# Optimization experiments

Hardware: AMD Instinct MI355X
Metric: run time of the kernel (lower is better)

The kernel has to match this reference:

```python
import jax, jax.numpy as jnp
import numpy as np

NUM_HEADS = 16
DIM_HEAD = 64
DIM = 1024
SCALE = DIM ** (-0.5)  # NOTE: source scales by model dim, not dim_head


def setup_inputs() -> dict:
    key = jax.random.key(0)
    ks = jax.random.split(key, 6)
    b, n, d = 2, 2048, DIM
    return {
        "x": jax.random.normal(ks[0], (b, n, d), dtype=jnp.float32),
        "mask": jnp.ones((b, n), dtype=bool),
        "Wq": jax.random.normal(ks[1], (NUM_HEADS * DIM_HEAD, d), dtype=jnp.float32) * 0.02,
        "Wk": jax.random.normal(ks[2], (DIM_HEAD, d), dtype=jnp.float32) * 0.02,
        "Wv": jax.random.normal(ks[3], (DIM_HEAD, d), dtype=jnp.float32) * 0.02,
        "Wfc": jax.random.normal(ks[4], (d, NUM_HEADS * DIM_HEAD), dtype=jnp.float32) * 0.02,
        "bfc": jnp.zeros((d,), dtype=jnp.float32),
    }


def reference(x, mask, Wq, Wk, Wv, Wfc, bfc):
    b, n, _ = x.shape
    # projections (nn.Linear: y = x @ W.T)
    q = (x @ Wq.T).reshape(b, n, NUM_HEADS, DIM_HEAD).transpose(0, 2, 1, 3)  # b h n d
    k = x @ Wk.T  # b n d  (single shared MQA head)
    v = x @ Wv.T  # b n d
    energy = jnp.einsum("bhid,bjd->bhij", q, k) * SCALE  # b h i j
    mask_value = -jnp.finfo(energy.dtype).max
    # input mask: k_mask is all ones in source, so only query rows are masked
    q_mask = mask[:, None, :, None]  # b 1 i 1
    energy = jnp.where(q_mask, energy, mask_value)
    # causal mask: positions j > i are masked (i == j since self-attention)
    i = jnp.arange(n)
    causal = i[:, None] < i[None, :]  # True where future
    energy = jnp.where(causal[None, None, :, :], mask_value, energy)
    attn = jax.nn.softmax(energy, axis=-1)
    # dropout_rate = 0.0 -> identity
    out = jnp.einsum("bhij,bjd->bhid", attn, v)
    out = out.transpose(0, 2, 1, 3).reshape(b, n, NUM_HEADS * DIM_HEAD)
    return out @ Wfc.T + bfc
```

## Files before the change

### kernel.cpp

```cpp
#include <hip/hip_runtime.h>
#include <math.h>

#define NH 16
#define DH 64
#define DM 1024
#define NS 2048
#define BB 2
#define MR (BB * NS)
#define LDQ 1152
#define C_EXP 0.0450842201f

typedef unsigned short u16;
typedef __attribute__((ext_vector_type(8))) short short8;
typedef __attribute__((ext_vector_type(4))) float floatx4;
typedef __attribute__((ext_vector_type(4))) u16 u16x4;

#if __has_builtin(__builtin_amdgcn_exp2f)
#define EXP2(x) __builtin_amdgcn_exp2f(x)
#else
#define EXP2(x) exp2f(x)
#endif

static __device__ __forceinline__ u16 f2bf(float f) {
  union { float f; unsigned u; } v; v.f = f;
  unsigned r = v.u + 0x7fffu + ((v.u >> 16) & 1u);
  return (u16)(r >> 16);
}
static __device__ __forceinline__ u16 f2bf_fast(float f) {
  union { float f; unsigned u; } v; v.f = f;
  return (u16)((v.u + 0x8000u) >> 16);
}

#define GLDS16(gp, lp)                                                        \
  __builtin_amdgcn_global_load_lds(                                           \
      (const __attribute__((address_space(1))) void*)(const void*)(gp),       \
      (__attribute__((address_space(3))) void*)(void*)(lp), 16, 0, 0)

__global__ __launch_bounds__(256) void cast_all(
    const float* __restrict__ x, const float* __restrict__ wq,
    const float* __restrict__ wk, const float* __restrict__ wv,
    const float* __restrict__ wfc, u16* __restrict__ xb,
    u16* __restrict__ wqkvb, u16* __restrict__ wfcb) {
  const int NX = MR * DM / 4, NQ = DM * DM / 4, NK = DH * DM / 4;
  int id = blockIdx.x * 256 + threadIdx.x;
  const float* src;
  u16* dst;
  int off;
  if (id < NX) { src = x; dst = xb; off = id; }
  else if (id < NX + NQ) { src = wq; dst = wqkvb; off = id - NX; }
  else if (id < NX + NQ + NK) { src = wk; dst = wqkvb + (size_t)DM * DM; off = id - NX - NQ; }
  else if (id < NX + NQ + 2 * NK) { src = wv; dst = wqkvb + (size_t)(DM + DH) * DM; off = id - NX - NQ - NK; }
  else { src = wfc; dst = wfcb; off = id - NX - NQ - 2 * NK; }
  float4 f = ((const float4*)src)[off];
  u16x4 o;
  o[0] = f2bf(f.x); o[1] = f2bf(f.y); o[2] = f2bf(f.z); o[3] = f2bf(f.w);
  ((u16x4*)dst)[off] = o;
}

__global__ __launch_bounds__(64) void gemm_bf16(
    const u16* __restrict__ A, const u16* __restrict__ W,
    const float* __restrict__ bias, void* __restrict__ Cout,
    u16* __restrict__ vT, int M, int N, int K, int ldc, int out_bf16,
    int v_bx) {
  __shared__ u16 As[2][64 * 32];
  __shared__ u16 Ws[2][64 * 32];
  const int lane = threadIdx.x;
  const int lr = lane & 15, quad = lane >> 4;
  const int m0 = blockIdx.y * 64, n0 = blockIdx.x * 64;

  const u16* gA[4];
  const u16* gW[4];
#pragma unroll
  for (int g = 0; g < 4; ++g) {
    int ci = g * 64 + lane;
    int row = ci >> 2;
    int cg = (ci & 3) ^ ((row >> 1) & 3);
    gA[g] = A + (size_t)(m0 + row) * K + cg * 8;
    gW[g] = W + (size_t)(n0 + row) * K + cg * 8;
  }

  floatx4 acc[4][4] = {};
  const int nt = K >> 5;

#pragma unroll
  for (int g = 0; g < 4; ++g) GLDS16(gA[g], &As[0][g * 512]);
#pragma unroll
  for (int g = 0; g < 4; ++g) GLDS16(gW[g], &Ws[0][g * 512]);

  for (int t = 0; t < nt; ++t) {
    if (t + 1 < nt) {
      const int ko = (t + 1) << 5;
      const int nb = (t + 1) & 1;
#pragma unroll
      for (int g = 0; g < 4; ++g) GLDS16(gA[g] + ko, &As[nb][g * 512]);
#pragma unroll
      for (int g = 0; g < 4; ++g) GLDS16(gW[g] + ko, &Ws[nb][g * 512]);
      asm volatile("s_waitcnt vmcnt(8)" ::: "memory");
    } else {
      asm volatile("s_waitcnt vmcnt(0)" ::: "memory");
    }
    const u16* as = As[t & 1];
    const u16* ws = Ws[t & 1];
    short8 af[4], wf[4];
#pragma unroll
    for (int mi = 0; mi < 4; ++mi) {
      int rr = mi * 16 + lr;
      af[mi] = *(const short8*)&as[rr * 32 + ((quad ^ ((rr >> 1) & 3)) << 3)];
    }
#pragma unroll
    for (int nj = 0; nj < 4; ++nj) {
      int rc = nj * 16 + lr;
      wf[nj] = *(const short8*)&ws[rc * 32 + ((quad ^ ((rc >> 1) & 3)) << 3)];
    }
#pragma unroll
    for (int mi = 0; mi < 4; ++mi)
#pragma unroll
      for (int nj = 0; nj < 4; ++nj)
        acc[mi][nj] = __builtin_amdgcn_mfma_f32_16x16x32_bf16(
            af[mi], wf[nj], acc[mi][nj], 0, 0, 0);
  }

  if (vT && blockIdx.x == v_bx) {
#pragma unroll
    for (int mi = 0; mi < 4; ++mi)
#pragma unroll
      for (int nj = 0; nj < 4; ++nj)
#pragma unroll
        for (int r = 0; r < 4; ++r)
          vT[(size_t)(nj * 16 + lr) * MR + m0 + mi * 16 + quad * 4 + r] =
              f2bf(acc[mi][nj][r]);
    return;
  }

#pragma unroll
  for (int mi = 0; mi < 4; ++mi) {
#pragma unroll
    for (int nj = 0; nj < 4; ++nj) {
      int col = n0 + nj * 16 + lr;
      float badd = bias ? bias[col] : 0.f;
#pragma unroll
      for (int r = 0; r < 4; ++r) {
        int row = m0 + mi * 16 + quad * 4 + r;
        float v = acc[mi][nj][r] + badd;
        if (out_bf16)
          ((u16*)Cout)[(size_t)row * ldc + col] = f2bf(v);
        else
          ((float*)Cout)[(size_t)row * ldc + col] = v;
      }
    }
  }
}

__global__ __launch_bounds__(128) void attn_mfma(
    const u16* __restrict__ qkv,
    const u16* __restrict__ vT,
    u16* __restrict__ aob) {
  __shared__ u16 Ks[2][64 * 64];
  __shared__ u16 Vt[2][64 * 64];
  __shared__ u16 Ps[2][16 * 72];

  const int b = blockIdx.z;
  const int p = blockIdx.x;
  const int head = blockIdx.y;
  const int tid = threadIdx.x;
  const int lane = tid & 63;
  const int lr = lane & 15, quad = lane >> 4;
  const int w = tid >> 6;
  const size_t rowb = (size_t)b * NS;
  const u16* kvK = qkv + rowb * LDQ + 1024;
  const u16* vTb = vT + rowb;

  int srow[4], scg[4];
#pragma unroll
  for (int g = 0; g < 4; ++g) {
    int ci = w * 256 + g * 64 + lane;
    srow[g] = ci >> 3;
    scg[g] = (ci & 7) ^ (srow[g] & 7);
  }

  for (int phase = 0; phase < 2; ++phase) {
    const int s = (phase == 0) ? (63 - p) : p;
    const int i0q = s * 32;
    const int ntp = (s >> 1) + 1;
    const int irow = i0q + w * 16 + quad * 4;

    const u16* qp = qkv + (rowb + i0q + w * 16 + lr) * LDQ + head * DH;
    short8 aq0 = *(const short8*)(qp + quad * 8);
    short8 aq1 = *(const short8*)(qp + 32 + quad * 8);

    floatx4 o[4] = {};
    float lacc[4] = {0.f, 0.f, 0.f, 0.f};

#pragma unroll
    for (int g = 0; g < 4; ++g)
      GLDS16(kvK + (size_t)srow[g] * LDQ + scg[g] * 8,
             &Ks[0][(w * 256 + g * 64) * 8]);
#pragma unroll
    for (int g = 0; g < 4; ++g)
      GLDS16(vTb + (size_t)srow[g] * MR + scg[g] * 8,
             &Vt[0][(w * 256 + g * 64) * 8]);

    for (int t = 0; t < ntp; ++t) {
      const int buf = t & 1;
      __syncthreads();

      if (t + 1 < ntp) {
        const int j0n = (t + 1) * 64;
        const int nb2 = buf ^ 1;
#pragma unroll
        for (int g = 0; g < 4; ++g)
          GLDS16(kvK + (size_t)(j0n + srow[g]) * LDQ + scg[g] * 8,
                 &Ks[nb2][(w * 256 + g * 64) * 8]);
#pragma unroll
        for (int g = 0; g < 4; ++g)
          GLDS16(vTb + (size_t)srow[g] * MR + j0n + scg[g] * 8,
                 &Vt[nb2][(w * 256 + g * 64) * 8]);
      }

      const int j0 = t * 64;
      const u16* ksb = Ks[buf];
      const u16* vtb = Vt[buf];
      floatx4 sv[4];
#pragma unroll
      for (int jb = 0; jb < 4; ++jb) {
        const int krow = jb * 16 + lr;
        short8 bk0 = *(const short8*)&ksb[krow * 64 + ((quad ^ (krow & 7)) << 3)];
        short8 bk1 = *(const short8*)&ksb[krow * 64 + (((4 + quad) ^ (krow & 7)) << 3)];
        floatx4 z = {};
        z = __builtin_amdgcn_mfma_f32_16x16x32_bf16(aq0, bk0, z, 0, 0, 0);
        z = __builtin_amdgcn_mfma_f32_16x16x32_bf16(aq1, bk1, z, 0, 0, 0);
        sv[jb] = z;
      }

      u16* Pw = Ps[w];
      const bool lastt = (t == ntp - 1);
#pragma unroll
      for (int jb = 0; jb < 4; ++jb) {
#pragma unroll
        for (int r = 0; r < 4; ++r) {
          float pe = EXP2(sv[jb][r] * C_EXP);
          if (lastt && (j0 + jb * 16 + lr > irow + r)) pe = 0.f;
          lacc[r] += pe;
          const int row = quad * 4 + r, colj = jb * 16 + lr;
          Pw[row * 72 + ((((colj >> 3) + (row >> 1)) & 7) << 3) + (colj & 7)] =
              f2bf_fast(pe);
        }
      }
      asm volatile("s_waitcnt lgkmcnt(0)" ::: "memory");
      short8 ap0 = *(const short8*)&Pw[lr * 72 + (((quad + (lr >> 1)) & 7) << 3)];
      short8 ap1 = *(const short8*)&Pw[lr * 72 + (((4 + quad + (lr >> 1)) & 7) << 3)];

#pragma unroll
      for (int nb = 0; nb < 4; ++nb) {
        const int d0 = nb * 16 + lr;
        short8 bv0 = *(const short8*)&vtb[d0 * 64 + ((quad ^ (d0 & 7)) << 3)];
        short8 bv1 = *(const short8*)&vtb[d0 * 64 + (((4 + quad) ^ (d0 & 7)) << 3)];
        o[nb] = __builtin_amdgcn_mfma_f32_16x16x32_bf16(ap0, bv0, o[nb], 0, 0, 0);
        o[nb] = __builtin_amdgcn_mfma_f32_16x16x32_bf16(ap1, bv1, o[nb], 0, 0, 0);
      }
    }

#pragma unroll
    for (int r = 0; r < 4; ++r) {
      float l = lacc[r];
      l += __shfl_xor(l, 1);
      l += __shfl_xor(l, 2);
      l += __shfl_xor(l, 4);
      l += __shfl_xor(l, 8);
      lacc[r] = l;
    }
#pragma unroll
    for (int nb = 0; nb < 4; ++nb)
#pragma unroll
      for (int r = 0; r < 4; ++r)
        aob[(rowb + irow + r) * DM + head * DH + nb * 16 + lr] =
            f2bf(o[nb][r] / lacc[r]);

    __syncthreads();
  }
}

extern "C" void kernel_launch(void* const* d_in, const int* in_sizes, int n_in,
                              void* d_out, int out_size, void* d_ws, size_t ws_size,
                              hipStream_t stream) {
  const float* x = (const float*)d_in[0];
  const float* Wq = (const float*)d_in[2];
  const float* Wk = (const float*)d_in[3];
  const float* Wv = (const float*)d_in[4];
  const float* Wfc = (const float*)d_in[5];
  const float* bfc = (const float*)d_in[6];

  u16* xb = (u16*)d_ws;
  u16* wqkvb = xb + (size_t)MR * DM;
  u16* wfcb = wqkvb + (size_t)LDQ * DM;
  u16* qkv = wfcb + (size_t)DM * DM;
  u16* vT = qkv + (size_t)MR * LDQ;
  u16* aob = xb;

  cast_all<<<dim3((MR * DM + DM * DM * 2 + DH * DM * 2) / 1024), dim3(256), 0,
             stream>>>(x, Wq, Wk, Wv, Wfc, xb, wqkvb, wfcb);
  gemm_bf16<<<dim3(LDQ / 64, MR / 64), dim3(64), 0, stream>>>(
      xb, wqkvb, nullptr, qkv, vT, MR, LDQ, DM, LDQ, 1, 17);
  attn_mfma<<<dim3(32, NH, BB), dim3(128), 0, stream>>>(qkv, vT, aob);
  gemm_bf16<<<dim3(DM / 64, MR / 64), dim3(64), 0, stream>>>(
      aob, wfcb, bfc, d_out, nullptr, MR, DM, DM, DM, 0, -1);
}
```

Baseline: 185.8 us.

## Load GEMM and attention operands directly from global into registers, bypassing LDS

Both GEMM kernels now load MFMA fragments straight from global memory into registers, using a two-step register double buffer instead of LDS staging with global_load_lds. The grid is also transposed so consecutive blocks walk along M. The attention kernel becomes one wave per block handling 32 query rows, and reads K and V^T fragments directly from global, keeping LDS only for the P tile. This removes LDS traffic and barriers but relies on the caches to serve repeated K/V and weight reads, so loads become uncoalesced, 16-byte-per-lane strided accesses.

```diff
diff --git a/kernel.cpp b/kernel.cpp
--- a/kernel.cpp
+++ b/kernel.cpp
@@ -21,6 +21,8 @@
 #define EXP2(x) exp2f(x)
 #endif
 
+#define MFMA16(a, b, c) __builtin_amdgcn_mfma_f32_16x16x32_bf16((a), (b), (c), 0, 0, 0)
+
 static __device__ __forceinline__ u16 f2bf(float f) {
   union { float f; unsigned u; } v; v.f = f;
   unsigned r = v.u + 0x7fffu + ((v.u >> 16) & 1u);
@@ -30,11 +32,6 @@
   union { float f; unsigned u; } v; v.f = f;
   return (u16)((v.u + 0x8000u) >> 16);
 }
-
-#define GLDS16(gp, lp)                                                        \
-  __builtin_amdgcn_global_load_lds(                                           \
-      (const __attribute__((address_space(1))) void*)(const void*)(gp),       \
-      (__attribute__((address_space(3))) void*)(void*)(lp), 16, 0, 0)
 
 __global__ __launch_bounds__(256) void cast_all(
     const float* __restrict__ x, const float* __restrict__ wq,
@@ -57,70 +54,57 @@
   ((u16x4*)dst)[off] = o;
 }
 
-__global__ __launch_bounds__(64) void gemm_bf16(
+__global__ __launch_bounds__(64) void gemm_dl(
     const u16* __restrict__ A, const u16* __restrict__ W,
     const float* __restrict__ bias, void* __restrict__ Cout,
     u16* __restrict__ vT, int M, int N, int K, int ldc, int out_bf16,
-    int v_bx) {
-  __shared__ u16 As[2][64 * 32];
-  __shared__ u16 Ws[2][64 * 32];
+    int v_by) {
   const int lane = threadIdx.x;
   const int lr = lane & 15, quad = lane >> 4;
-  const int m0 = blockIdx.y * 64, n0 = blockIdx.x * 64;
-
-  const u16* gA[4];
-  const u16* gW[4];
-#pragma unroll
-  for (int g = 0; g < 4; ++g) {
-    int ci = g * 64 + lane;
-    int row = ci >> 2;
-    int cg = (ci & 3) ^ ((row >> 1) & 3);
-    gA[g] = A + (size_t)(m0 + row) * K + cg * 8;
-    gW[g] = W + (size_t)(n0 + row) * K + cg * 8;
-  }
-
+  const int m0 = blockIdx.x * 64, n0 = blockIdx.y * 64;
+
+  const u16* gA = A + (size_t)(m0 + lr) * K + quad * 8;
+  const u16* gW = W + (size_t)(n0 + lr) * K + quad * 8;
+
+  short8 afA[4], afB[4], wf[4];
   floatx4 acc[4][4] = {};
+
+#pragma unroll
+  for (int i = 0; i < 4; ++i) {
+    afA[i] = *(const short8*)(gA + (size_t)i * 16 * K);
+    wf[i] = *(const short8*)(gW + (size_t)i * 16 * K);
+  }
+
   const int nt = K >> 5;
-
-#pragma unroll
-  for (int g = 0; g < 4; ++g) GLDS16(gA[g], &As[0][g * 512]);
-#pragma unroll
-  for (int g = 0; g < 4; ++g) GLDS16(gW[g], &Ws[0][g * 512]);
-
-  for (int t = 0; t < nt; ++t) {
-    if (t + 1 < nt) {
-      const int ko = (t + 1) << 5;
-      const int nb = (t + 1) & 1;
-#pragma unroll
-      for (int g = 0; g < 4; ++g) GLDS16(gA[g] + ko, &As[nb][g * 512]);
-#pragma unroll
-      for (int g = 0; g < 4; ++g) GLDS16(gW[g] + ko, &Ws[nb][g * 512]);
-      asm volatile("s_waitcnt vmcnt(8)" ::: "memory");
-    } else {
-      asm volatile("s_waitcnt vmcnt(0)" ::: "memory");
-    }
-    const u16* as = As[t & 1];
-    const u16* ws = Ws[t & 1];
-    short8 af[4], wf[4];
-#pragma unroll
-    for (int mi = 0; mi < 4; ++mi) {
-      int rr = mi * 16 + lr;
-      af[mi] = *(const short8*)&as[rr * 32 + ((quad ^ ((rr >> 1) & 3)) << 3)];
-    }
+  for (int t = 0; t < nt; t += 2) {
+    const int k1 = (t + 1) << 5;
+    const int k2 = (t + 2) << 5;
+#pragma unroll
+    for (int i = 0; i < 4; ++i)
+      afB[i] = *(const short8*)(gA + (size_t)i * 16 * K + k1);
 #pragma unroll
     for (int nj = 0; nj < 4; ++nj) {
-      int rc = nj * 16 + lr;
-      wf[nj] = *(const short8*)&ws[rc * 32 + ((quad ^ ((rc >> 1) & 3)) << 3)];
-    }
-#pragma unroll
-    for (int mi = 0; mi < 4; ++mi)
-#pragma unroll
-      for (int nj = 0; nj < 4; ++nj)
-        acc[mi][nj] = __builtin_amdgcn_mfma_f32_16x16x32_bf16(
-            af[mi], wf[nj], acc[mi][nj], 0, 0, 0);
-  }
-
-  if (vT && blockIdx.x == v_bx) {
+#pragma unroll
+      for (int mi = 0; mi < 4; ++mi)
+        acc[mi][nj] = MFMA16(afA[mi], wf[nj], acc[mi][nj]);
+      wf[nj] = *(const short8*)(gW + (size_t)nj * 16 * K + k1);
+    }
+    const bool hn = (t + 2) < nt;
+    if (hn) {
+#pragma unroll
+      for (int i = 0; i < 4; ++i)
+        afA[i] = *(const short8*)(gA + (size_t)i * 16 * K + k2);
+    }
+#pragma unroll
+    for (int nj = 0; nj < 4; ++nj) {
+#pragma unroll
+      for (int mi = 0; mi < 4; ++mi)
+        acc[mi][nj] = MFMA16(afB[mi], wf[nj], acc[mi][nj]);
+      if (hn) wf[nj] = *(const short8*)(gW + (size_t)nj * 16 * K + k2);
+    }
+  }
+
+  if (v_by >= 0 && (int)blockIdx.y == v_by) {
 #pragma unroll
     for (int mi = 0; mi < 4; ++mi)
 #pragma unroll
@@ -151,132 +135,127 @@
   }
 }
 
-__global__ __launch_bounds__(128) void attn_mfma(
+__global__ __launch_bounds__(64) void attn_dl(
     const u16* __restrict__ qkv,
     const u16* __restrict__ vT,
     u16* __restrict__ aob) {
-  __shared__ u16 Ks[2][64 * 64];
-  __shared__ u16 Vt[2][64 * 64];
-  __shared__ u16 Ps[2][16 * 72];
-
-  const int b = blockIdx.z;
-  const int p = blockIdx.x;
-  const int head = blockIdx.y;
-  const int tid = threadIdx.x;
-  const int lane = tid & 63;
+  __shared__ u16 Ps[2][32 * 72];
+
+  const int b = blockIdx.z, p = blockIdx.x, head = blockIdx.y;
+  const int lane = threadIdx.x;
   const int lr = lane & 15, quad = lane >> 4;
-  const int w = tid >> 6;
   const size_t rowb = (size_t)b * NS;
-  const u16* kvK = qkv + rowb * LDQ + 1024;
-  const u16* vTb = vT + rowb;
-
-  int srow[4], scg[4];
-#pragma unroll
-  for (int g = 0; g < 4; ++g) {
-    int ci = w * 256 + g * 64 + lane;
-    srow[g] = ci >> 3;
-    scg[g] = (ci & 7) ^ (srow[g] & 7);
-  }
+  const u16* kp = qkv + (rowb + lr) * LDQ + 1024;
+  const u16* vp = vT + rowb + (size_t)lr * MR;
 
   for (int phase = 0; phase < 2; ++phase) {
     const int s = (phase == 0) ? (63 - p) : p;
     const int i0q = s * 32;
     const int ntp = (s >> 1) + 1;
-    const int irow = i0q + w * 16 + quad * 4;
-
-    const u16* qp = qkv + (rowb + i0q + w * 16 + lr) * LDQ + head * DH;
-    short8 aq0 = *(const short8*)(qp + quad * 8);
-    short8 aq1 = *(const short8*)(qp + 32 + quad * 8);
-
-    floatx4 o[4] = {};
-    float lacc[4] = {0.f, 0.f, 0.f, 0.f};
-
-#pragma unroll
-    for (int g = 0; g < 4; ++g)
-      GLDS16(kvK + (size_t)srow[g] * LDQ + scg[g] * 8,
-             &Ks[0][(w * 256 + g * 64) * 8]);
-#pragma unroll
-    for (int g = 0; g < 4; ++g)
-      GLDS16(vTb + (size_t)srow[g] * MR + scg[g] * 8,
-             &Vt[0][(w * 256 + g * 64) * 8]);
+
+    short8 aq[2][2];
+#pragma unroll
+    for (int g = 0; g < 2; ++g) {
+      const u16* qp = qkv + (rowb + i0q + g * 16 + lr) * LDQ + head * DH;
+      aq[g][0] = *(const short8*)(qp + quad * 8);
+      aq[g][1] = *(const short8*)(qp + 32 + quad * 8);
+    }
+
+    floatx4 o[2][4] = {};
+    float lacc[2][4] = {};
+    short8 kf[8], vf[8];
+
+#pragma unroll
+    for (int jb = 0; jb < 4; ++jb) {
+      kf[2 * jb] = *(const short8*)(kp + (size_t)(jb * 16) * LDQ + quad * 8);
+      kf[2 * jb + 1] = *(const short8*)(kp + (size_t)(jb * 16) * LDQ + 32 + quad * 8);
+    }
 
     for (int t = 0; t < ntp; ++t) {
-      const int buf = t & 1;
-      __syncthreads();
+      const int j0 = t * 64;
+#pragma unroll
+      for (int nb = 0; nb < 4; ++nb) {
+        vf[2 * nb] = *(const short8*)(vp + (size_t)(nb * 16) * MR + j0 + quad * 8);
+        vf[2 * nb + 1] = *(const short8*)(vp + (size_t)(nb * 16) * MR + j0 + 32 + quad * 8);
+      }
+
+      floatx4 sv[2][4];
+#pragma unroll
+      for (int jb = 0; jb < 4; ++jb) {
+        floatx4 z0 = {}, z1 = {};
+        z0 = MFMA16(aq[0][0], kf[2 * jb], z0);
+        z0 = MFMA16(aq[0][1], kf[2 * jb + 1], z0);
+        z1 = MFMA16(aq[1][0], kf[2 * jb], z1);
+        z1 = MFMA16(aq[1][1], kf[2 * jb + 1], z1);
+        sv[0][jb] = z0;
+        sv[1][jb] = z1;
+      }
 
       if (t + 1 < ntp) {
-        const int j0n = (t + 1) * 64;
-        const int nb2 = buf ^ 1;
-#pragma unroll
-        for (int g = 0; g < 4; ++g)
-          GLDS16(kvK + (size_t)(j0n + srow[g]) * LDQ + scg[g] * 8,
-                 &Ks[nb2][(w * 256 + g * 64) * 8]);
-#pragma unroll
-        for (int g = 0; g < 4; ++g)
-          GLDS16(vTb + (size_t)srow[g] * MR + j0n + scg[g] * 8,
-                 &Vt[nb2][(w * 256 + g * 64) * 8]);
-      }
-
-      const int j0 = t * 64;
-      const u16* ksb = Ks[buf];
-      const u16* vtb = Vt[buf];
-      floatx4 sv[4];
-#pragma unroll
-      for (int jb = 0; jb < 4; ++jb) {
-        const int krow = jb * 16 + lr;
-        short8 bk0 = *(const short8*)&ksb[krow * 64 + ((quad ^ (krow & 7)) << 3)];
-        short8 bk1 = *(const short8*)&ksb[krow * 64 + (((4 + quad) ^ (krow & 7)) << 3)];
-        floatx4 z = {};
-        z = __builtin_amdgcn_mfma_f32_16x16x32_bf16(aq0, bk0, z, 0, 0, 0);
-        z = __builtin_amdgcn_mfma_f32_16x16x32_bf16(aq1, bk1, z, 0, 0, 0);
-        sv[jb] = z;
-      }
-
-      u16* Pw = Ps[w];
+        const int j0n = j0 + 64;
+#pragma unroll
+        for (int jb = 0; jb < 4; ++jb) {
+          kf[2 * jb] = *(const short8*)(kp + (size_t)(j0n + jb * 16) * LDQ + quad * 8);
+          kf[2 * jb + 1] = *(const short8*)(kp + (size_t)(j0n + jb * 16) * LDQ + 32 + quad * 8);
+        }
+      }
+
+      u16* Pw = Ps[t & 1];
       const bool lastt = (t == ntp - 1);
 #pragma unroll
-      for (int jb = 0; jb < 4; ++jb) {
+      for (int g = 0; g < 2; ++g) {
+        const int irow = i0q + g * 16 + quad * 4;
+#pragma unroll
+        for (int jb = 0; jb < 4; ++jb)
+#pragma unroll
+          for (int r = 0; r < 4; ++r) {
+            float pe = EXP2(sv[g][jb][r] * C_EXP);
+            if (lastt && (j0 + jb * 16 + lr > irow + r)) pe = 0.f;
+            lacc[g][r] += pe;
+            const int row = g * 16 + quad * 4 + r, colj = jb * 16 + lr;
+            Pw[row * 72 + ((((colj >> 3) + (row >> 1)) & 7) << 3) + (colj & 7)] =
+                f2bf_fast(pe);
+          }
+      }
+      asm volatile("s_waitcnt lgkmcnt(0)" ::: "memory");
+      short8 ap[2][2];
+#pragma unroll
+      for (int g = 0; g < 2; ++g) {
+        const int row = g * 16 + lr;
+        ap[g][0] = *(const short8*)&Pw[row * 72 + (((quad + (row >> 1)) & 7) << 3)];
+        ap[g][1] = *(const short8*)&Pw[row * 72 + (((4 + quad + (row >> 1)) & 7) << 3)];
+      }
+
+#pragma unroll
+      for (int nb = 0; nb < 4; ++nb)
+#pragma unroll
+        for (int g = 0; g < 2; ++g) {
+          o[g][nb] = MFMA16(ap[g][0], vf[2 * nb], o[g][nb]);
+          o[g][nb] = MFMA16(ap[g][1], vf[2 * nb + 1], o[g][nb]);
+        }
+    }
+
+#pragma unroll
+    for (int g = 0; g < 2; ++g)
+#pragma unroll
+      for (int r = 0; r < 4; ++r) {
+        float l = lacc[g][r];
+        l += __shfl_xor(l, 1);
+        l += __shfl_xor(l, 2);
+        l += __shfl_xor(l, 4);
+        l += __shfl_xor(l, 8);
+        lacc[g][r] = l;
+      }
+#pragma unroll
+    for (int g = 0; g < 2; ++g)
+#pragma unroll
+      for (int nb = 0; nb < 4; ++nb)
 #pragma unroll
         for (int r = 0; r < 4; ++r) {
-          float pe = EXP2(sv[jb][r] * C_EXP);
-          if (lastt && (j0 + jb * 16 + lr > irow + r)) pe = 0.f;
-          lacc[r] += pe;
-          const int row = quad * 4 + r, colj = jb * 16 + lr;
-          Pw[row * 72 + ((((colj >> 3) + (row >> 1)) & 7) << 3) + (colj & 7)] =
-              f2bf_fast(pe);
+          const int row = i0q + g * 16 + quad * 4 + r;
+          aob[(rowb + row) * DM + head * DH + nb * 16 + lr] =
+              f2bf(o[g][nb][r] / lacc[g][r]);
         }
-      }
-      asm volatile("s_waitcnt lgkmcnt(0)" ::: "memory");
-      short8 ap0 = *(const short8*)&Pw[lr * 72 + (((quad + (lr >> 1)) & 7) << 3)];
-      short8 ap1 = *(const short8*)&Pw[lr * 72 + (((4 + quad + (lr >> 1)) & 7) << 3)];
-
-#pragma unroll
-      for (int nb = 0; nb < 4; ++nb) {
-        const int d0 = nb * 16 + lr;
-        short8 bv0 = *(const short8*)&vtb[d0 * 64 + ((quad ^ (d0 & 7)) << 3)];
-        short8 bv1 = *(const short8*)&vtb[d0 * 64 + (((4 + quad) ^ (d0 & 7)) << 3)];
-        o[nb] = __builtin_amdgcn_mfma_f32_16x16x32_bf16(ap0, bv0, o[nb], 0, 0, 0);
-        o[nb] = __builtin_amdgcn_mfma_f32_16x16x32_bf16(ap1, bv1, o[nb], 0, 0, 0);
-      }
-    }
-
-#pragma unroll
-    for (int r = 0; r < 4; ++r) {
-      float l = lacc[r];
-      l += __shfl_xor(l, 1);
-      l += __shfl_xor(l, 2);
-      l += __shfl_xor(l, 4);
-      l += __shfl_xor(l, 8);
-      lacc[r] = l;
-    }
-#pragma unroll
-    for (int nb = 0; nb < 4; ++nb)
-#pragma unroll
-      for (int r = 0; r < 4; ++r)
-        aob[(rowb + irow + r) * DM + head * DH + nb * 16 + lr] =
-            f2bf(o[nb][r] / lacc[r]);
-
-    __syncthreads();
   }
 }
 
@@ -299,9 +278,9 @@
 
   cast_all<<<dim3((MR * DM + DM * DM * 2 + DH * DM * 2) / 1024), dim3(256), 0,
              stream>>>(x, Wq, Wk, Wv, Wfc, xb, wqkvb, wfcb);
-  gemm_bf16<<<dim3(LDQ / 64, MR / 64), dim3(64), 0, stream>>>(
+  gemm_dl<<<dim3(MR / 64, LDQ / 64), dim3(64), 0, stream>>>(
       xb, wqkvb, nullptr, qkv, vT, MR, LDQ, DM, LDQ, 1, 17);
-  attn_mfma<<<dim3(32, NH, BB), dim3(128), 0, stream>>>(qkv, vT, aob);
-  gemm_bf16<<<dim3(DM / 64, MR / 64), dim3(64), 0, stream>>>(
+  attn_dl<<<dim3(32, NH, BB), dim3(64), 0, stream>>>(qkv, vT, aob);
+  gemm_dl<<<dim3(MR / 64, DM / 64), dim3(64), 0, stream>>>(
       aob, wfcb, bfc, d_out, nullptr, MR, DM, DM, DM, 0, -1);
 }
```

After: 240.2 us. 1.29x slower.

## Split GEMM 64x64 tile across four waves and swap grid axes

Applied to the files above, without the earlier changes.

The projection GEMM kernel now uses 256 threads (four waves) per 64x64 output tile. Each wave computes a 32x32 quadrant, and each thread issues one async global-to-LDS load per operand per K-step, in place of one wave doing everything. The grid now walks M along x and N along y, which changes the block scheduling order so neighbouring blocks share weight tiles. This lowers per-wave register pressure and raises wave-level parallelism, but adds a __syncthreads per K iteration and relies on the barrier for completion of the async loads.

```diff
diff --git a/kernel.cpp b/kernel.cpp
--- a/kernel.cpp
+++ b/kernel.cpp
@@ -20,6 +20,8 @@
 #else
 #define EXP2(x) exp2f(x)
 #endif
+
+#define MFMA16(a, b, c) __builtin_amdgcn_mfma_f32_16x16x32_bf16((a), (b), (c), 0, 0, 0)
 
 static __device__ __forceinline__ u16 f2bf(float f) {
   union { float f; unsigned u; } v; v.f = f;
@@ -57,90 +59,80 @@
   ((u16x4*)dst)[off] = o;
 }
 
-__global__ __launch_bounds__(64) void gemm_bf16(
+__global__ __launch_bounds__(256) void gemm64(
     const u16* __restrict__ A, const u16* __restrict__ W,
     const float* __restrict__ bias, void* __restrict__ Cout,
     u16* __restrict__ vT, int M, int N, int K, int ldc, int out_bf16,
-    int v_bx) {
+    int v_by) {
   __shared__ u16 As[2][64 * 32];
   __shared__ u16 Ws[2][64 * 32];
-  const int lane = threadIdx.x;
+  const int tid = threadIdx.x;
+  const int lane = tid & 63;
   const int lr = lane & 15, quad = lane >> 4;
-  const int m0 = blockIdx.y * 64, n0 = blockIdx.x * 64;
-
-  const u16* gA[4];
-  const u16* gW[4];
-#pragma unroll
-  for (int g = 0; g < 4; ++g) {
-    int ci = g * 64 + lane;
-    int row = ci >> 2;
-    int cg = (ci & 3) ^ ((row >> 1) & 3);
-    gA[g] = A + (size_t)(m0 + row) * K + cg * 8;
-    gW[g] = W + (size_t)(n0 + row) * K + cg * 8;
-  }
-
-  floatx4 acc[4][4] = {};
+  const int wave = tid >> 6, wr = wave >> 1, wc = wave & 1;
+  const int m0 = blockIdx.x * 64, n0 = blockIdx.y * 64;
+
+  const int srow = tid >> 2;
+  const int scg = (tid & 3) ^ ((srow >> 1) & 3);
+  const u16* gA = A + (size_t)(m0 + srow) * K + scg * 8;
+  const u16* gW = W + (size_t)(n0 + srow) * K + scg * 8;
+  const int lo = wave * 512;
+
+  floatx4 acc[2][2] = {};
   const int nt = K >> 5;
 
-#pragma unroll
-  for (int g = 0; g < 4; ++g) GLDS16(gA[g], &As[0][g * 512]);
-#pragma unroll
-  for (int g = 0; g < 4; ++g) GLDS16(gW[g], &Ws[0][g * 512]);
+  GLDS16(gA, &As[0][lo]);
+  GLDS16(gW, &Ws[0][lo]);
 
   for (int t = 0; t < nt; ++t) {
+    __syncthreads();
     if (t + 1 < nt) {
       const int ko = (t + 1) << 5;
       const int nb = (t + 1) & 1;
-#pragma unroll
-      for (int g = 0; g < 4; ++g) GLDS16(gA[g] + ko, &As[nb][g * 512]);
-#pragma unroll
-      for (int g = 0; g < 4; ++g) GLDS16(gW[g] + ko, &Ws[nb][g * 512]);
-      asm volatile("s_waitcnt vmcnt(8)" ::: "memory");
-    } else {
-      asm volatile("s_waitcnt vmcnt(0)" ::: "memory");
+      GLDS16(gA + ko, &As[nb][lo]);
+      GLDS16(gW + ko, &Ws[nb][lo]);
     }
     const u16* as = As[t & 1];
     const u16* ws = Ws[t & 1];
-    short8 af[4], wf[4];
-#pragma unroll
-    for (int mi = 0; mi < 4; ++mi) {
-      int rr = mi * 16 + lr;
+    short8 af[2], wf[2];
+#pragma unroll
+    for (int mi = 0; mi < 2; ++mi) {
+      int rr = wr * 32 + mi * 16 + lr;
       af[mi] = *(const short8*)&as[rr * 32 + ((quad ^ ((rr >> 1) & 3)) << 3)];
     }
 #pragma unroll
-    for (int nj = 0; nj < 4; ++nj) {
-      int rc = nj * 16 + lr;
+    for (int nj = 0; nj < 2; ++nj) {
+      int rc = wc * 32 + nj * 16 + lr;
       wf[nj] = *(const short8*)&ws[rc * 32 + ((quad ^ ((rc >> 1) & 3)) << 3)];
     }
 #pragma unroll
-    for (int mi = 0; mi < 4; ++mi)
-#pragma unroll
-      for (int nj = 0; nj < 4; ++nj)
-        acc[mi][nj] = __builtin_amdgcn_mfma_f32_16x16x32_bf16(
-            af[mi], wf[nj], acc[mi][nj], 0, 0, 0);
-  }
-
-  if (vT && blockIdx.x == v_bx) {
-#pragma unroll
-    for (int mi = 0; mi < 4; ++mi)
-#pragma unroll
-      for (int nj = 0; nj < 4; ++nj)
+    for (int mi = 0; mi < 2; ++mi)
+#pragma unroll
+      for (int nj = 0; nj < 2; ++nj)
+        acc[mi][nj] = MFMA16(af[mi], wf[nj], acc[mi][nj]);
+  }
+
+  if (v_by >= 0 && (int)blockIdx.y == v_by) {
+#pragma unroll
+    for (int mi = 0; mi < 2; ++mi)
+#pragma unroll
+      for (int nj = 0; nj < 2; ++nj)
 #pragma unroll
         for (int r = 0; r < 4; ++r)
-          vT[(size_t)(nj * 16 + lr) * MR + m0 + mi * 16 + quad * 4 + r] =
-              f2bf(acc[mi][nj][r]);
+          vT[(size_t)(wc * 32 + nj * 16 + lr) * MR + m0 + wr * 32 + mi * 16 +
+             quad * 4 + r] = f2bf(acc[mi][nj][r]);
     return;
   }
 
 #pragma unroll
-  for (int mi = 0; mi < 4; ++mi) {
-#pragma unroll
-    for (int nj = 0; nj < 4; ++nj) {
-      int col = n0 + nj * 16 + lr;
+  for (int mi = 0; mi < 2; ++mi) {
+#pragma unroll
+    for (int nj = 0; nj < 2; ++nj) {
+      int col = n0 + wc * 32 + nj * 16 + lr;
       float badd = bias ? bias[col] : 0.f;
 #pragma unroll
       for (int r = 0; r < 4; ++r) {
-        int row = m0 + mi * 16 + quad * 4 + r;
+        int row = m0 + wr * 32 + mi * 16 + quad * 4 + r;
         float v = acc[mi][nj][r] + badd;
         if (out_bf16)
           ((u16*)Cout)[(size_t)row * ldc + col] = f2bf(v);
@@ -227,8 +219,8 @@
         short8 bk0 = *(const short8*)&ksb[krow * 64 + ((quad ^ (krow & 7)) << 3)];
         short8 bk1 = *(const short8*)&ksb[krow * 64 + (((4 + quad) ^ (krow & 7)) << 3)];
         floatx4 z = {};
-        z = __builtin_amdgcn_mfma_f32_16x16x32_bf16(aq0, bk0, z, 0, 0, 0);
-        z = __builtin_amdgcn_mfma_f32_16x16x32_bf16(aq1, bk1, z, 0, 0, 0);
+        z = MFMA16(aq0, bk0, z);
+        z = MFMA16(aq1, bk1, z);
         sv[jb] = z;
       }
 
@@ -255,8 +247,8 @@
         const int d0 = nb * 16 + lr;
         short8 bv0 = *(const short8*)&vtb[d0 * 64 + ((quad ^ (d0 & 7)) << 3)];
         short8 bv1 = *(const short8*)&vtb[d0 * 64 + (((4 + quad) ^ (d0 & 7)) << 3)];
-        o[nb] = __builtin_amdgcn_mfma_f32_16x16x32_bf16(ap0, bv0, o[nb], 0, 0, 0);
-        o[nb] = __builtin_amdgcn_mfma_f32_16x16x32_bf16(ap1, bv1, o[nb], 0, 0, 0);
+        o[nb] = MFMA16(ap0, bv0, o[nb]);
+        o[nb] = MFMA16(ap1, bv1, o[nb]);
       }
     }
 
@@ -299,9 +291,9 @@
 
   cast_all<<<dim3((MR * DM + DM * DM * 2 + DH * DM * 2) / 1024), dim3(256), 0,
              stream>>>(x, Wq, Wk, Wv, Wfc, xb, wqkvb, wfcb);
-  gemm_bf16<<<dim3(LDQ / 64, MR / 64), dim3(64), 0, stream>>>(
+  gemm64<<<dim3(MR / 64, LDQ / 64), dim3(256), 0, stream>>>(
       xb, wqkvb, nullptr, qkv, vT, MR, LDQ, DM, LDQ, 1, 17);
   attn_mfma<<<dim3(32, NH, BB), dim3(128), 0, stream>>>(qkv, vT, aob);
-  gemm_bf16<<<dim3(DM / 64, MR / 64), dim3(64), 0, stream>>>(
+  gemm64<<<dim3(MR / 64, DM / 64), dim3(256), 0, stream>>>(
       aob, wfcb, bfc, d_out, nullptr, MR, DM, DM, DM, 0, -1);
 }
```

After: 168.4 us. 9.4% less time.
